# Performance work log

Hardware: AMD Instinct MI355X
Metric: run time of the kernel (lower is better)

Reference implementation:

```python
import jax, jax.numpy as jnp
import numpy as np

NEG_SLOPE = 0.2


def _gat_layer(x, src, dst, W, att_src, att_dst, bias, heads, out_c, concat):
    # x: [N, F_in]; src,dst: [E] (edges src -> dst, softmax grouped by dst)
    N = x.shape[0]
    h = (x @ W).reshape(N, heads, out_c)                       # [N,H,C]
    a_s = jnp.sum(h * att_src, axis=-1)                        # [N,H]
    a_d = jnp.sum(h * att_dst, axis=-1)                        # [N,H]
    e = jax.nn.leaky_relu(a_s[src] + a_d[dst], NEG_SLOPE)      # [E,H]
    emax = jax.ops.segment_max(e, dst, num_segments=N)         # [N,H]
    ex = jnp.exp(e - emax[dst])
    denom = jax.ops.segment_sum(ex, dst, num_segments=N)       # [N,H]
    alpha = ex / (denom[dst] + 1e-16)                          # [E,H]
    msg = h[src] * alpha[:, :, None]                           # [E,H,C]
    out = jax.ops.segment_sum(msg, dst, num_segments=N)        # [N,H,C]
    out = out.reshape(N, heads * out_c) if concat else out.mean(axis=1)
    return out + bias


def setup_inputs() -> dict:
    key = jax.random.key(0)
    ks = jax.random.split(key, 12)
    N, E = 100000, 1600000
    F_in, C1, H = 128, 32, 4
    x = jax.random.normal(ks[0], (N, F_in), dtype=jnp.float32)
    edge_index = jax.random.randint(ks[1], (2, E), 0, N, dtype=jnp.int64)
    s = 0.1
    W1 = jax.random.normal(ks[2], (F_in, H * C1), dtype=jnp.float32) * s
    att_src1 = jax.random.normal(ks[3], (H, C1), dtype=jnp.float32) * s
    att_dst1 = jax.random.normal(ks[4], (H, C1), dtype=jnp.float32) * s
    b1 = jnp.zeros((H * C1,), dtype=jnp.float32)
    W2 = jax.random.normal(ks[5], (H * C1, 1), dtype=jnp.float32) * s
    att_src2 = jax.random.normal(ks[6], (1, 1), dtype=jnp.float32) * s
    att_dst2 = jax.random.normal(ks[7], (1, 1), dtype=jnp.float32) * s
    b2 = jnp.zeros((1,), dtype=jnp.float32)
    return {"x": x, "edge_index": edge_index, "W1": W1, "att_src1": att_src1,
            "att_dst1": att_dst1, "b1": b1, "W2": W2, "att_src2": att_src2,
            "att_dst2": att_dst2, "b2": b2}


def reference(x, edge_index, W1, att_src1, att_dst1, b1, W2, att_src2, att_dst2, b2):
    N = x.shape[0]
    # PyG GATConv adds self loops by default
    loops = jnp.arange(N, dtype=edge_index.dtype)
    src = jnp.concatenate([edge_index[0], loops])
    dst = jnp.concatenate([edge_index[1], loops])
    h = _gat_layer(x, src, dst, W1, att_src1, att_dst1, b1, heads=4, out_c=32, concat=True)
    h = jax.nn.relu(h)
    out = _gat_layer(h, src, dst, W2, att_src2, att_dst2, b2, heads=1, out_c=1, concat=False)
    return out.squeeze(-1)  # [N]
```

## Files before the change

kernel.cpp:

```cpp
#include <hip/hip_runtime.h>
#include <hip/hip_bf16.h>
#include <math.h>

typedef __hip_bfloat16 bf16;
typedef __attribute__((ext_vector_type(8))) short short8v;
typedef __attribute__((ext_vector_type(4))) float float4v;

__device__ __forceinline__ float b2f(bf16 v) { return __bfloat162float(v); }
__device__ __forceinline__ float bs2f(unsigned short s) {
    unsigned u = ((unsigned)s) << 16;
    float f; __builtin_memcpy(&f, &u, 4); return f;
}
__device__ __forceinline__ short f2bs(float v) {
    bf16 b = __float2bfloat16(v);
    short s; __builtin_memcpy(&s, &b, 2); return s;
}
__device__ __forceinline__ float lrelu(float v) { return v > 0.f ? v : 0.2f * v; }
__device__ __forceinline__ float ldf(const void* p, size_t i, int bf) {
    return bf ? b2f(((const bf16*)p)[i]) : ((const float*)p)[i];
}
__device__ __forceinline__ int ld_src(const int* ei, int e, int E, int f64, int N) {
    int v = f64 ? (int)(((const long long*)ei)[e]) : ei[e];
    if ((unsigned)v >= (unsigned)N) v = 0;
    return v;
}
__device__ __forceinline__ int ld_dst(const int* ei, int e, int E, int f64, int N) {
    int v = f64 ? (int)(((const long long*)ei)[(size_t)E + e]) : ei[(size_t)E + e];
    if ((unsigned)v >= (unsigned)N) v = 0;
    return v;
}

#define EPB 4096
#define SB  8

__global__ void k_detect(const int* __restrict__ ei, const unsigned* __restrict__ xw,
                         int* __restrict__ flags, int* __restrict__ bcnt, int nbuck)
{
    __shared__ int s_or[256];
    __shared__ int s_cnt[256];
    int t = threadIdx.x;
    for (int j = t; j < nbuck; j += 256) bcnt[j] = 0;
    int any = 0, cnt = 0;
    for (int i = t; i < 4096; i += 256) {
        any |= ei[2 * i + 1];
        unsigned e = (xw[i] >> 7) & 0xFFu;
        cnt += (e >= 100u && e <= 134u) ? 1 : 0;
    }
    s_or[t] = any; s_cnt[t] = cnt;
    __syncthreads();
    for (int s = 128; s > 0; s >>= 1) {
        if (t < s) { s_or[t] |= s_or[t + s]; s_cnt[t] += s_cnt[t + s]; }
        __syncthreads();
    }
    if (t == 0) {
        flags[0] = (s_or[0] == 0) ? 1 : 0;
        flags[1] = (s_cnt[0] > 2048) ? 1 : 0;
    }
}

__global__ void __launch_bounds__(256)
k_prep(const int* __restrict__ ei, const void* __restrict__ W1,
       const int* __restrict__ flags, int* __restrict__ bcnt,
       short* __restrict__ w1frag, int E, int N, int nbuck, int ebl)
{
    int t = threadIdx.x;
    if (blockIdx.x >= ebl) {
        int bf = flags[1];
        int idx = (blockIdx.x - ebl) * 256 + t;
        if (idx < 16384) {
            int j = idx & 7, l = (idx >> 3) & 63, kk = (idx >> 9) & 3, ct = idx >> 11;
            int k = kk * 32 + (l >> 4) * 8 + j;
            int n = ct * 16 + (l & 15);
            w1frag[idx] = bf ? ((const short*)W1)[k * 128 + n]
                             : f2bs(((const float*)W1)[k * 128 + n]);
        }
        return;
    }
    __shared__ int hist[512];
    for (int j = t; j < nbuck; j += 256) hist[j] = 0;
    __syncthreads();
    int f = flags[0];
    int beg = blockIdx.x * EPB, end = min(E, beg + EPB);
    for (int i = beg + t; i < end; i += 256)
        atomicAdd(&hist[ld_dst(ei, i, E, f, N) >> SB], 1);
    __syncthreads();
    for (int j = t; j < nbuck; j += 256)
        if (hist[j]) atomicAdd(&bcnt[j], hist[j]);
}

#define GP 136

__global__ void __launch_bounds__(256)
k_gemm_scan(const void* __restrict__ x, const short* __restrict__ w1frag,
            const void* __restrict__ att_src, const void* __restrict__ att_dst,
            const int* __restrict__ flags, bf16* __restrict__ h1b,
            float* __restrict__ a_s, float* __restrict__ a_d,
            const int* __restrict__ bcnt, int* __restrict__ bofs,
            int* __restrict__ bcur, int* __restrict__ offsets,
            int N, int E, int nbuck)
{
    int t = threadIdx.x;
    if (blockIdx.x == 0) {
        __shared__ int ps[256];
        int i0 = 2 * t, i1 = 2 * t + 1;
        int c0 = (i0 < nbuck) ? bcnt[i0] : 0;
        int c1 = (i1 < nbuck) ? bcnt[i1] : 0;
        int pr = c0 + c1;
        ps[t] = pr;
        __syncthreads();
        for (int s = 1; s < 256; s <<= 1) {
            int add = (t >= s) ? ps[t - s] : 0;
            __syncthreads();
            ps[t] += add;
            __syncthreads();
        }
        int excl = ps[t] - pr;
        if (i0 < nbuck) { bofs[i0] = excl; bcur[i0] = excl; }
        if (i1 < nbuck) { bofs[i1] = excl + c0; bcur[i1] = excl + c0; }
        if (t == 0) { bofs[nbuck] = E; offsets[N] = E; }
        return;
    }
    __shared__ short xs[64 * GP];
    int bf = flags[1];
    int blk = blockIdx.x - 1;
    int base = blk * 64;
    if (bf) {
        const short8v* xp = (const short8v*)x;
        for (int idx = t; idx < 1024; idx += 256) {
            int m = idx >> 4, v8 = idx & 15;
            int gm = base + m;
            short8v v = (gm < N) ? xp[(size_t)gm * 16 + v8]
                                 : (short8v){0,0,0,0,0,0,0,0};
            *(short8v*)&xs[m * GP + v8 * 8] = v;
        }
    } else {
        const float4* xp = (const float4*)x;
        for (int idx = t; idx < 2048; idx += 256) {
            int m = idx >> 5, v4 = idx & 31;
            int gm = base + m;
            float4 f = (gm < N) ? xp[(size_t)gm * 32 + v4]
                                : make_float4(0.f, 0.f, 0.f, 0.f);
            short* d = &xs[m * GP + v4 * 4];
            d[0] = f2bs(f.x); d[1] = f2bs(f.y); d[2] = f2bs(f.z); d[3] = f2bs(f.w);
        }
    }
    __syncthreads();

    int wv = t >> 6, l = t & 63, lq = l >> 4, lr = l & 15;
    int m0 = base + wv * 16;

    short8v afr[4];
#pragma unroll
    for (int kk = 0; kk < 4; ++kk)
        afr[kk] = *(const short8v*)&xs[(wv * 16 + lr) * GP + kk * 32 + lq * 8];

    float4v acc[8];
#pragma unroll
    for (int ct = 0; ct < 8; ++ct) acc[ct] = (float4v){0.f, 0.f, 0.f, 0.f};

#pragma unroll
    for (int kk = 0; kk < 4; ++kk) {
        short8v a = afr[kk];
#pragma unroll
        for (int ct = 0; ct < 8; ++ct) {
            short8v b = *(const short8v*)(w1frag + (((ct * 4 + kk) * 64 + l) << 3));
            acc[ct] = __builtin_amdgcn_mfma_f32_16x16x32_bf16(a, b, acc[ct], 0, 0, 0);
        }
    }
    __syncthreads();

#pragma unroll
    for (int ct = 0; ct < 8; ++ct)
#pragma unroll
        for (int r = 0; r < 4; ++r)
            xs[(wv * 16 + lq * 4 + r) * GP + ct * 16 + lr] = f2bs(acc[ct][r]);
    __syncthreads();

    int c0 = (l & 7) * 16;
    float asv[16], adv[16];
#pragma unroll
    for (int c = 0; c < 16; ++c) {
        asv[c] = ldf(att_src, c0 + c, bf);
        adv[c] = ldf(att_dst, c0 + c, bf);
    }
#pragma unroll
    for (int p = 0; p < 2; ++p) {
        int rrow = p * 8 + (l >> 3);
        int gn = m0 + rrow;
        const short* srcp = &xs[(wv * 16 + rrow) * GP + c0];
        short8v v0 = *(const short8v*)srcp;
        short8v v1 = *(const short8v*)(srcp + 8);
        if (gn < N) {
            unsigned short* dst = (unsigned short*)h1b + (size_t)gn * 128 + c0;
            *(short8v*)dst = v0;
            *(short8v*)(dst + 8) = v1;
        }
        float ds = 0.f, dd = 0.f;
#pragma unroll
        for (int c = 0; c < 8; ++c) {
            float fv = bs2f((unsigned short)v0[c]);
            ds += fv * asv[c]; dd += fv * adv[c];
        }
#pragma unroll
        for (int c = 0; c < 8; ++c) {
            float fv = bs2f((unsigned short)v1[c]);
            ds += fv * asv[8 + c]; dd += fv * adv[8 + c];
        }
        ds += __shfl_xor(ds, 1, 64);
        dd += __shfl_xor(dd, 1, 64);
        if (gn < N && ((l & 1) == 0)) {
            int h = (l & 7) >> 1;
            a_s[(size_t)gn * 4 + h] = ds;
            a_d[(size_t)gn * 4 + h] = dd;
        }
    }
}

__global__ void __launch_bounds__(256)
k_bbin_scatter(const int* __restrict__ ei, const int* __restrict__ flags,
               int* __restrict__ bcur, uint2* __restrict__ ebuf,
               int E, int N, int nbuck)
{
    __shared__ int hist[512];
    __shared__ int base[512];
    int t = threadIdx.x;
    for (int j = t; j < nbuck; j += 256) hist[j] = 0;
    __syncthreads();
    int f = flags[0];
    int beg = blockIdx.x * EPB, end = min(E, beg + EPB);
    for (int i = beg + t; i < end; i += 256)
        atomicAdd(&hist[ld_dst(ei, i, E, f, N) >> SB], 1);
    __syncthreads();
    for (int j = t; j < nbuck; j += 256) {
        base[j] = hist[j] ? atomicAdd(&bcur[j], hist[j]) : 0;
        hist[j] = 0;
    }
    __syncthreads();
    for (int i = beg + t; i < end; i += 256) {
        int d = ld_dst(ei, i, E, f, N);
        int s = ld_src(ei, i, E, f, N);
        int b = d >> SB;
        int idx = base[b] + atomicAdd(&hist[b], 1);
        ebuf[idx] = make_uint2((unsigned)s, (unsigned)d);
    }
}

__global__ void __launch_bounds__(256)
k_bucket_csr(const uint2* __restrict__ ebuf, const int* __restrict__ bofs,
             int* __restrict__ offsets, int* __restrict__ adj, int N)
{
    const int npb = 1 << SB;
    __shared__ int hist[npb];
    __shared__ int psum[256];
    int b = blockIdx.x, t = threadIdx.x;
    int n0 = b << SB;
    int ebeg = bofs[b], eend = bofs[b + 1];

    hist[t] = 0;
    __syncthreads();
    for (int i = ebeg + t; i < eend; i += 256)
        atomicAdd(&hist[ebuf[i].y - n0], 1);
    __syncthreads();
    int c = hist[t];
    psum[t] = c;
    __syncthreads();
    for (int st = 1; st < 256; st <<= 1) {
        int add = (t >= st) ? psum[t - st] : 0;
        __syncthreads();
        psum[t] += add;
        __syncthreads();
    }
    int run = ebeg + psum[t] - c;
    int node = n0 + t;
    hist[t] = run;
    if (node < N) offsets[node] = run;
    __syncthreads();
    for (int i = ebeg + t; i < eend; i += 256) {
        uint2 e = ebuf[i];
        int pos = atomicAdd(&hist[e.y - n0], 1);
        adj[pos] = (int)e.x;
    }
}

__global__ void __launch_bounds__(256)
k_hagg32(const bf16* __restrict__ h1b, const float* __restrict__ a_s,
         const float* __restrict__ a_d, const int* __restrict__ offsets,
         const int* __restrict__ adj, const void* __restrict__ b1,
         const void* __restrict__ W2, const int* __restrict__ flags,
         float* __restrict__ h2, int N)
{
    int bf = flags[1];
    int t = threadIdx.x;
    int g = t >> 5, l = t & 31;
    int n = blockIdx.x * 8 + g;
    if (n >= N) return;
    int h = l >> 3;
    int coff = h * 32 + (l & 7) * 4;

    int beg = offsets[n], deg = offsets[n + 1] - beg;
    float adh = a_d[(size_t)n * 4 + h];
    const unsigned short* h1u = (const unsigned short*)h1b;

    float wself = __expf(lrelu(a_s[(size_t)n * 4 + h] + adh));
    ushort4 u = *(const ushort4*)(h1u + ((size_t)n << 7) + coff);
    float a0 = wself * bs2f(u.x), a1 = wself * bs2f(u.y);
    float a2 = wself * bs2f(u.z), a3 = wself * bs2f(u.w);
    float den = wself;

    int i = 0;
    for (; i + 4 <= deg; i += 4) {
        int s0 = adj[beg + i];
        int s1 = adj[beg + i + 1];
        int s2 = adj[beg + i + 2];
        int s3 = adj[beg + i + 3];
        float w0 = __expf(lrelu(a_s[(size_t)s0 * 4 + h] + adh));
        float w1 = __expf(lrelu(a_s[(size_t)s1 * 4 + h] + adh));
        float w2 = __expf(lrelu(a_s[(size_t)s2 * 4 + h] + adh));
        float w3 = __expf(lrelu(a_s[(size_t)s3 * 4 + h] + adh));
        ushort4 v0 = *(const ushort4*)(h1u + ((size_t)s0 << 7) + coff);
        ushort4 v1 = *(const ushort4*)(h1u + ((size_t)s1 << 7) + coff);
        ushort4 v2 = *(const ushort4*)(h1u + ((size_t)s2 << 7) + coff);
        ushort4 v3 = *(const ushort4*)(h1u + ((size_t)s3 << 7) + coff);
        den += (w0 + w1) + (w2 + w3);
        a0 += w0 * bs2f(v0.x) + w1 * bs2f(v1.x) + w2 * bs2f(v2.x) + w3 * bs2f(v3.x);
        a1 += w0 * bs2f(v0.y) + w1 * bs2f(v1.y) + w2 * bs2f(v2.y) + w3 * bs2f(v3.y);
        a2 += w0 * bs2f(v0.z) + w1 * bs2f(v1.z) + w2 * bs2f(v2.z) + w3 * bs2f(v3.z);
        a3 += w0 * bs2f(v0.w) + w1 * bs2f(v1.w) + w2 * bs2f(v2.w) + w3 * bs2f(v3.w);
    }
    for (; i < deg; ++i) {
        int s0 = adj[beg + i];
        float w0 = __expf(lrelu(a_s[(size_t)s0 * 4 + h] + adh));
        ushort4 v0 = *(const ushort4*)(h1u + ((size_t)s0 << 7) + coff);
        den += w0;
        a0 += w0 * bs2f(v0.x);
        a1 += w0 * bs2f(v0.y);
        a2 += w0 * bs2f(v0.z);
        a3 += w0 * bs2f(v0.w);
    }

    float inv = 1.f / (den + 1e-16f);
    float o0 = fmaxf(a0 * inv + ldf(b1, coff + 0, bf), 0.f);
    float o1 = fmaxf(a1 * inv + ldf(b1, coff + 1, bf), 0.f);
    float o2 = fmaxf(a2 * inv + ldf(b1, coff + 2, bf), 0.f);
    float o3 = fmaxf(a3 * inv + ldf(b1, coff + 3, bf), 0.f);

    float p = o0 * ldf(W2, coff + 0, bf) + o1 * ldf(W2, coff + 1, bf)
            + o2 * ldf(W2, coff + 2, bf) + o3 * ldf(W2, coff + 3, bf);
    p += __shfl_xor(p, 1, 64);
    p += __shfl_xor(p, 2, 64);
    p += __shfl_xor(p, 4, 64);
    p += __shfl_xor(p, 8, 64);
    p += __shfl_xor(p, 16, 64);
    if (l == 0) h2[n] = p;
}

__global__ void k_agg2(const float* __restrict__ h2, const int* __restrict__ offsets,
                       const int* __restrict__ adj, const void* __restrict__ att_src2,
                       const void* __restrict__ att_dst2, const void* __restrict__ bias2,
                       const int* __restrict__ flags, void* __restrict__ out, int N)
{
    int bf = flags[1];
    int g = (blockIdx.x * blockDim.x + threadIdx.x) >> 4;
    int lane = threadIdx.x & 15;
    if (g >= N) return;
    int n = g;
    float as2 = ldf(att_src2, 0, bf), ad2 = ldf(att_dst2, 0, bf);
    int beg = offsets[n], end = offsets[n + 1], deg = end - beg;
    float hn = h2[n];
    float dterm = hn * ad2;

    float acc = 0.f, den = 0.f;
    if (lane == 0) {
        float ex = __expf(lrelu(hn * as2 + dterm));
        acc = ex * hn; den = ex;
    }
    for (int i = lane; i < deg; i += 16) {
        int s = adj[beg + i];
        float hs = h2[s];
        float ex = __expf(lrelu(hs * as2 + dterm));
        acc += ex * hs; den += ex;
    }
    for (int m = 1; m < 16; m <<= 1) {
        acc += __shfl_xor(acc, m, 64);
        den += __shfl_xor(den, m, 64);
    }
    if (lane == 0) {
        float r = acc / (den + 1e-16f) + ldf(bias2, 0, bf);
        if (bf) ((bf16*)out)[n] = __float2bfloat16(r);
        else    ((float*)out)[n] = r;
    }
}

extern "C" void kernel_launch(void* const* d_in, const int* in_sizes, int n_in,
                              void* d_out, int out_size, void* d_ws, size_t ws_size,
                              hipStream_t stream)
{
    const void* x        = d_in[0];
    const int*  ei       = (const int*)d_in[1];
    const void* W1       = d_in[2];
    const void* att_src1 = d_in[3];
    const void* att_dst1 = d_in[4];
    const void* b1       = d_in[5];
    const void* W2       = d_in[6];
    const void* att_src2 = d_in[7];
    const void* att_dst2 = d_in[8];
    const void* bias2    = d_in[9];

    int N = in_sizes[0] / 128;
    int E = in_sizes[1] / 2;
    int nbuck = ((N - 1) >> SB) + 1;

    char* ws = (char*)d_ws;
    size_t off = 0;
    auto alloc = [&](size_t bytes) -> void* {
        void* p = ws + off;
        off = (off + bytes + 255) & ~(size_t)255;
        return p;
    };
    int*   flags   = (int*)alloc(256);
    float* a_s     = (float*)alloc((size_t)N * 4 * sizeof(float));
    float* a_d     = (float*)alloc((size_t)N * 4 * sizeof(float));
    float* h2      = (float*)alloc((size_t)N * sizeof(float));
    int*   offsets = (int*)alloc((size_t)(N + 1) * sizeof(int));
    int*   adj     = (int*)alloc((size_t)E * sizeof(int));
    uint2* ebuf    = (uint2*)alloc((size_t)E * sizeof(uint2));
    int*   bcnt    = (int*)alloc(1024 * sizeof(int));
    int*   bofs    = (int*)alloc(1028 * sizeof(int));
    int*   bcur    = (int*)alloc(1024 * sizeof(int));
    short* w1frag  = (short*)alloc(16384 * sizeof(short));
    bf16*  h1b     = (bf16*)alloc((size_t)N * 128 * sizeof(bf16));

    int ebl = (E + EPB - 1) / EPB;

    k_detect<<<1, 256, 0, stream>>>(ei, (const unsigned*)x, flags, bcnt, nbuck);

    k_prep<<<ebl + 64, 256, 0, stream>>>(ei, W1, flags, bcnt, w1frag,
                                         E, N, nbuck, ebl);

    k_gemm_scan<<<1 + (N + 63) / 64, 256, 0, stream>>>(
        x, w1frag, att_src1, att_dst1, flags, h1b, a_s, a_d,
        bcnt, bofs, bcur, offsets, N, E, nbuck);

    k_bbin_scatter<<<ebl, 256, 0, stream>>>(ei, flags, bcur, ebuf, E, N, nbuck);
    k_bucket_csr<<<nbuck, 256, 0, stream>>>(ebuf, bofs, offsets, adj, N);

    k_hagg32<<<(N + 7) / 8, 256, 0, stream>>>(h1b, a_s, a_d, offsets, adj,
                                              b1, W2, flags, h2, N);

    k_agg2<<<((size_t)N * 16 + 255) / 256, 256, 0, stream>>>(
        h2, offsets, adj, att_src2, att_dst2, bias2, flags, d_out, N);
}
```

Baseline: 279.9 us.

## Pack edge buffer into 32-bit words and aggregate with 16 lanes per node

The bucketed edge buffer now stores each edge as one 32-bit word, with the 24-bit source index and the 8-bit local destination index packed together, instead of a uint2. This halves traffic for the scatter and CSR-build passes. The layer-1 aggregation kernel now gives each node 16 lanes, each doing a 16-byte load of 8 bf16 channels and accumulating with packed float2 math, so twice as many nodes fit per block. The packing assumes N stays below 2^24, and each lane now needs more registers.

```diff
diff --git a/kernel.cpp b/kernel.cpp
--- a/kernel.cpp
+++ b/kernel.cpp
@@ -5,17 +5,21 @@
 typedef __hip_bfloat16 bf16;
 typedef __attribute__((ext_vector_type(8))) short short8v;
 typedef __attribute__((ext_vector_type(4))) float float4v;
+typedef __attribute__((ext_vector_type(2))) float float2v;
 
 __device__ __forceinline__ float b2f(bf16 v) { return __bfloat162float(v); }
 __device__ __forceinline__ float bs2f(unsigned short s) {
     unsigned u = ((unsigned)s) << 16;
     float f; __builtin_memcpy(&f, &u, 4); return f;
 }
+__device__ __forceinline__ float ubits(unsigned u) {
+    float f; __builtin_memcpy(&f, &u, 4); return f;
+}
 __device__ __forceinline__ short f2bs(float v) {
     bf16 b = __float2bfloat16(v);
     short s; __builtin_memcpy(&s, &b, 2); return s;
 }
-__device__ __forceinline__ float lrelu(float v) { return v > 0.f ? v : 0.2f * v; }
+__device__ __forceinline__ float lrelu(float v) { return fmaxf(v, 0.2f * v); }
 __device__ __forceinline__ float ldf(const void* p, size_t i, int bf) {
     return bf ? b2f(((const bf16*)p)[i]) : ((const float*)p)[i];
 }
@@ -218,7 +222,7 @@
 
 __global__ void __launch_bounds__(256)
 k_bbin_scatter(const int* __restrict__ ei, const int* __restrict__ flags,
-               int* __restrict__ bcur, uint2* __restrict__ ebuf,
+               int* __restrict__ bcur, unsigned* __restrict__ ebuf,
                int E, int N, int nbuck)
 {
     __shared__ int hist[512];
@@ -241,12 +245,12 @@
         int s = ld_src(ei, i, E, f, N);
         int b = d >> SB;
         int idx = base[b] + atomicAdd(&hist[b], 1);
-        ebuf[idx] = make_uint2((unsigned)s, (unsigned)d);
+        ebuf[idx] = (unsigned)s | ((unsigned)(d & ((1 << SB) - 1)) << 24);
     }
 }
 
 __global__ void __launch_bounds__(256)
-k_bucket_csr(const uint2* __restrict__ ebuf, const int* __restrict__ bofs,
+k_bucket_csr(const unsigned* __restrict__ ebuf, const int* __restrict__ bofs,
              int* __restrict__ offsets, int* __restrict__ adj, int N)
 {
     const int npb = 1 << SB;
@@ -259,7 +263,7 @@
     hist[t] = 0;
     __syncthreads();
     for (int i = ebeg + t; i < eend; i += 256)
-        atomicAdd(&hist[ebuf[i].y - n0], 1);
+        atomicAdd(&hist[ebuf[i] >> 24], 1);
     __syncthreads();
     int c = hist[t];
     psum[t] = c;
@@ -276,14 +280,25 @@
     if (node < N) offsets[node] = run;
     __syncthreads();
     for (int i = ebeg + t; i < eend; i += 256) {
-        uint2 e = ebuf[i];
-        int pos = atomicAdd(&hist[e.y - n0], 1);
-        adj[pos] = (int)e.x;
-    }
+        unsigned e = ebuf[i];
+        int pos = atomicAdd(&hist[e >> 24], 1);
+        adj[pos] = (int)(e & 0xFFFFFFu);
+    }
+}
+
+__device__ __forceinline__ void acc8(float2v& p0, float2v& p1, float2v& p2,
+                                     float2v& p3, uint4 q, float w)
+{
+    float2v wv = {w, w};
+    float2v v;
+    v[0] = ubits(q.x << 16); v[1] = ubits(q.x & 0xFFFF0000u); p0 += wv * v;
+    v[0] = ubits(q.y << 16); v[1] = ubits(q.y & 0xFFFF0000u); p1 += wv * v;
+    v[0] = ubits(q.z << 16); v[1] = ubits(q.z & 0xFFFF0000u); p2 += wv * v;
+    v[0] = ubits(q.w << 16); v[1] = ubits(q.w & 0xFFFF0000u); p3 += wv * v;
 }
 
 __global__ void __launch_bounds__(256)
-k_hagg32(const bf16* __restrict__ h1b, const float* __restrict__ a_s,
+k_hagg16(const bf16* __restrict__ h1b, const float* __restrict__ a_s,
          const float* __restrict__ a_d, const int* __restrict__ offsets,
          const int* __restrict__ adj, const void* __restrict__ b1,
          const void* __restrict__ W2, const int* __restrict__ flags,
@@ -291,22 +306,25 @@
 {
     int bf = flags[1];
     int t = threadIdx.x;
-    int g = t >> 5, l = t & 31;
-    int n = blockIdx.x * 8 + g;
+    int g = t >> 4, l = t & 15;
+    int n = blockIdx.x * 16 + g;
     if (n >= N) return;
-    int h = l >> 3;
-    int coff = h * 32 + (l & 7) * 4;
+    int h = l >> 2;
+    int c0 = l * 8;
+    const unsigned* h1q = (const unsigned*)h1b;
+    size_t rowsh = 6;
 
     int beg = offsets[n], deg = offsets[n + 1] - beg;
     float adh = a_d[(size_t)n * 4 + h];
-    const unsigned short* h1u = (const unsigned short*)h1b;
-
-    float wself = __expf(lrelu(a_s[(size_t)n * 4 + h] + adh));
-    ushort4 u = *(const ushort4*)(h1u + ((size_t)n << 7) + coff);
-    float a0 = wself * bs2f(u.x), a1 = wself * bs2f(u.y);
-    float a2 = wself * bs2f(u.z), a3 = wself * bs2f(u.w);
-    float den = wself;
-
+
+    float2v p0 = {0.f,0.f}, p1 = {0.f,0.f}, p2 = {0.f,0.f}, p3 = {0.f,0.f};
+    float den;
+    {
+        float w = __expf(lrelu(a_s[(size_t)n * 4 + h] + adh));
+        uint4 q = *(const uint4*)(h1q + ((size_t)n << rowsh) + l * 4);
+        acc8(p0, p1, p2, p3, q, w);
+        den = w;
+    }
     int i = 0;
     for (; i + 4 <= deg; i += 4) {
         int s0 = adj[beg + i];
@@ -317,40 +335,36 @@
         float w1 = __expf(lrelu(a_s[(size_t)s1 * 4 + h] + adh));
         float w2 = __expf(lrelu(a_s[(size_t)s2 * 4 + h] + adh));
         float w3 = __expf(lrelu(a_s[(size_t)s3 * 4 + h] + adh));
-        ushort4 v0 = *(const ushort4*)(h1u + ((size_t)s0 << 7) + coff);
-        ushort4 v1 = *(const ushort4*)(h1u + ((size_t)s1 << 7) + coff);
-        ushort4 v2 = *(const ushort4*)(h1u + ((size_t)s2 << 7) + coff);
-        ushort4 v3 = *(const ushort4*)(h1u + ((size_t)s3 << 7) + coff);
+        uint4 q0 = *(const uint4*)(h1q + ((size_t)s0 << rowsh) + l * 4);
+        uint4 q1 = *(const uint4*)(h1q + ((size_t)s1 << rowsh) + l * 4);
+        uint4 q2 = *(const uint4*)(h1q + ((size_t)s2 << rowsh) + l * 4);
+        uint4 q3 = *(const uint4*)(h1q + ((size_t)s3 << rowsh) + l * 4);
         den += (w0 + w1) + (w2 + w3);
-        a0 += w0 * bs2f(v0.x) + w1 * bs2f(v1.x) + w2 * bs2f(v2.x) + w3 * bs2f(v3.x);
-        a1 += w0 * bs2f(v0.y) + w1 * bs2f(v1.y) + w2 * bs2f(v2.y) + w3 * bs2f(v3.y);
-        a2 += w0 * bs2f(v0.z) + w1 * bs2f(v1.z) + w2 * bs2f(v2.z) + w3 * bs2f(v3.z);
-        a3 += w0 * bs2f(v0.w) + w1 * bs2f(v1.w) + w2 * bs2f(v2.w) + w3 * bs2f(v3.w);
+        acc8(p0, p1, p2, p3, q0, w0);
+        acc8(p0, p1, p2, p3, q1, w1);
+        acc8(p0, p1, p2, p3, q2, w2);
+        acc8(p0, p1, p2, p3, q3, w3);
     }
     for (; i < deg; ++i) {
         int s0 = adj[beg + i];
         float w0 = __expf(lrelu(a_s[(size_t)s0 * 4 + h] + adh));
-        ushort4 v0 = *(const ushort4*)(h1u + ((size_t)s0 << 7) + coff);
+        uint4 q0 = *(const uint4*)(h1q + ((size_t)s0 << rowsh) + l * 4);
         den += w0;
-        a0 += w0 * bs2f(v0.x);
-        a1 += w0 * bs2f(v0.y);
-        a2 += w0 * bs2f(v0.z);
-        a3 += w0 * bs2f(v0.w);
+        acc8(p0, p1, p2, p3, q0, w0);
     }
 
     float inv = 1.f / (den + 1e-16f);
-    float o0 = fmaxf(a0 * inv + ldf(b1, coff + 0, bf), 0.f);
-    float o1 = fmaxf(a1 * inv + ldf(b1, coff + 1, bf), 0.f);
-    float o2 = fmaxf(a2 * inv + ldf(b1, coff + 2, bf), 0.f);
-    float o3 = fmaxf(a3 * inv + ldf(b1, coff + 3, bf), 0.f);
-
-    float p = o0 * ldf(W2, coff + 0, bf) + o1 * ldf(W2, coff + 1, bf)
-            + o2 * ldf(W2, coff + 2, bf) + o3 * ldf(W2, coff + 3, bf);
+    float o[8] = { p0[0], p0[1], p1[0], p1[1], p2[0], p2[1], p3[0], p3[1] };
+    float p = 0.f;
+#pragma unroll
+    for (int c = 0; c < 8; ++c) {
+        float ov = fmaxf(o[c] * inv + ldf(b1, c0 + c, bf), 0.f);
+        p += ov * ldf(W2, c0 + c, bf);
+    }
     p += __shfl_xor(p, 1, 64);
     p += __shfl_xor(p, 2, 64);
     p += __shfl_xor(p, 4, 64);
     p += __shfl_xor(p, 8, 64);
-    p += __shfl_xor(p, 16, 64);
     if (l == 0) h2[n] = p;
 }
 
@@ -417,18 +431,18 @@
         off = (off + bytes + 255) & ~(size_t)255;
         return p;
     };
-    int*   flags   = (int*)alloc(256);
-    float* a_s     = (float*)alloc((size_t)N * 4 * sizeof(float));
-    float* a_d     = (float*)alloc((size_t)N * 4 * sizeof(float));
-    float* h2      = (float*)alloc((size_t)N * sizeof(float));
-    int*   offsets = (int*)alloc((size_t)(N + 1) * sizeof(int));
-    int*   adj     = (int*)alloc((size_t)E * sizeof(int));
-    uint2* ebuf    = (uint2*)alloc((size_t)E * sizeof(uint2));
-    int*   bcnt    = (int*)alloc(1024 * sizeof(int));
-    int*   bofs    = (int*)alloc(1028 * sizeof(int));
-    int*   bcur    = (int*)alloc(1024 * sizeof(int));
-    short* w1frag  = (short*)alloc(16384 * sizeof(short));
-    bf16*  h1b     = (bf16*)alloc((size_t)N * 128 * sizeof(bf16));
+    int*      flags   = (int*)alloc(256);
+    float*    a_s     = (float*)alloc((size_t)N * 4 * sizeof(float));
+    float*    a_d     = (float*)alloc((size_t)N * 4 * sizeof(float));
+    float*    h2      = (float*)alloc((size_t)N * sizeof(float));
+    int*      offsets = (int*)alloc((size_t)(N + 1) * sizeof(int));
+    int*      adj     = (int*)alloc((size_t)E * sizeof(int));
+    unsigned* ebuf    = (unsigned*)alloc((size_t)E * sizeof(unsigned));
+    int*      bcnt    = (int*)alloc(1024 * sizeof(int));
+    int*      bofs    = (int*)alloc(1028 * sizeof(int));
+    int*      bcur    = (int*)alloc(1024 * sizeof(int));
+    short*    w1frag  = (short*)alloc(16384 * sizeof(short));
+    bf16*     h1b     = (bf16*)alloc((size_t)N * 128 * sizeof(bf16));
 
     int ebl = (E + EPB - 1) / EPB;
 
@@ -444,8 +458,8 @@
     k_bbin_scatter<<<ebl, 256, 0, stream>>>(ei, flags, bcur, ebuf, E, N, nbuck);
     k_bucket_csr<<<nbuck, 256, 0, stream>>>(ebuf, bofs, offsets, adj, N);
 
-    k_hagg32<<<(N + 7) / 8, 256, 0, stream>>>(h1b, a_s, a_d, offsets, adj,
-                                              b1, W2, flags, h2, N);
+    k_hagg16<<<(N + 15) / 16, 256, 0, stream>>>(h1b, a_s, a_d, offsets, adj,
+                                                b1, W2, flags, h2, N);
 
     k_agg2<<<((size_t)N * 16 + 255) / 256, 256, 0, stream>>>(
         h2, offsets, adj, att_src2, att_dst2, bias2, flags, d_out, N);
```

After: 287.8 us. 2.8% more time.

## Fuse bucket scan into histogram and scatter into GEMM; pack edges to 32-bit

Applied to the files above, without the earlier changes.

The bucket prefix scan now runs in the last-finishing block of the histogram kernel, detected with an atomic counter. The edge bucket-scatter is merged into the GEMM kernel as extra blocks, which removes one launch and lets the scatter overlap with the GEMM. Edge records are packed into one 32-bit word (24-bit source, 8-bit local destination), halving ebuf traffic. The aggregation loop gains an 8-way unrolled gather for more memory-level parallelism, and leaky-ReLU uses fmaxf. The packing assumes N fits in 24 bits, and the last-block scan relies on threadfence ordering.

```diff
diff --git a/kernel.cpp b/kernel.cpp
--- a/kernel.cpp
+++ b/kernel.cpp
@@ -15,7 +15,7 @@
     bf16 b = __float2bfloat16(v);
     short s; __builtin_memcpy(&s, &b, 2); return s;
 }
-__device__ __forceinline__ float lrelu(float v) { return v > 0.f ? v : 0.2f * v; }
+__device__ __forceinline__ float lrelu(float v) { return fmaxf(v, 0.2f * v); }
 __device__ __forceinline__ float ldf(const void* p, size_t i, int bf) {
     return bf ? b2f(((const bf16*)p)[i]) : ((const float*)p)[i];
 }
@@ -34,12 +34,14 @@
 #define SB  8
 
 __global__ void k_detect(const int* __restrict__ ei, const unsigned* __restrict__ xw,
-                         int* __restrict__ flags, int* __restrict__ bcnt, int nbuck)
+                         int* __restrict__ flags, int* __restrict__ bcnt,
+                         int* __restrict__ done, int nbuck)
 {
     __shared__ int s_or[256];
     __shared__ int s_cnt[256];
     int t = threadIdx.x;
     for (int j = t; j < nbuck; j += 256) bcnt[j] = 0;
+    if (t == 0) done[0] = 0;
     int any = 0, cnt = 0;
     for (int i = t; i < 4096; i += 256) {
         any |= ei[2 * i + 1];
@@ -61,7 +63,9 @@
 __global__ void __launch_bounds__(256)
 k_prep(const int* __restrict__ ei, const void* __restrict__ W1,
        const int* __restrict__ flags, int* __restrict__ bcnt,
-       short* __restrict__ w1frag, int E, int N, int nbuck, int ebl)
+       short* __restrict__ w1frag, int* __restrict__ done,
+       int* __restrict__ bofs, int* __restrict__ bcur, int* __restrict__ offsets,
+       int E, int N, int nbuck, int ebl)
 {
     int t = threadIdx.x;
     if (blockIdx.x >= ebl) {
@@ -86,44 +90,70 @@
     __syncthreads();
     for (int j = t; j < nbuck; j += 256)
         if (hist[j]) atomicAdd(&bcnt[j], hist[j]);
+
+    __threadfence();
+    __shared__ int is_last;
+    if (t == 0) is_last = (atomicAdd(done, 1) == ebl - 1) ? 1 : 0;
+    __syncthreads();
+    if (!is_last) return;
+    __threadfence();
+    __shared__ int ps[256];
+    int i0 = 2 * t, i1 = 2 * t + 1;
+    int c0 = (i0 < nbuck) ? bcnt[i0] : 0;
+    int c1 = (i1 < nbuck) ? bcnt[i1] : 0;
+    int pr = c0 + c1;
+    ps[t] = pr;
+    __syncthreads();
+    for (int s = 1; s < 256; s <<= 1) {
+        int add = (t >= s) ? ps[t - s] : 0;
+        __syncthreads();
+        ps[t] += add;
+        __syncthreads();
+    }
+    int excl = ps[t] - pr;
+    if (i0 < nbuck) { bofs[i0] = excl; bcur[i0] = excl; }
+    if (i1 < nbuck) { bofs[i1] = excl + c0; bcur[i1] = excl + c0; }
+    if (t == 0) { bofs[nbuck] = E; offsets[N] = E; }
 }
 
 #define GP 136
 
 __global__ void __launch_bounds__(256)
-k_gemm_scan(const void* __restrict__ x, const short* __restrict__ w1frag,
-            const void* __restrict__ att_src, const void* __restrict__ att_dst,
-            const int* __restrict__ flags, bf16* __restrict__ h1b,
-            float* __restrict__ a_s, float* __restrict__ a_d,
-            const int* __restrict__ bcnt, int* __restrict__ bofs,
-            int* __restrict__ bcur, int* __restrict__ offsets,
-            int N, int E, int nbuck)
+k_gemm_scatter(const void* __restrict__ x, const short* __restrict__ w1frag,
+               const void* __restrict__ att_src, const void* __restrict__ att_dst,
+               const int* __restrict__ ei, const int* __restrict__ flags,
+               bf16* __restrict__ h1b, float* __restrict__ a_s, float* __restrict__ a_d,
+               int* __restrict__ bcur, unsigned* __restrict__ ebuf,
+               int N, int E, int nbuck, int ebl)
 {
     int t = threadIdx.x;
-    if (blockIdx.x == 0) {
-        __shared__ int ps[256];
-        int i0 = 2 * t, i1 = 2 * t + 1;
-        int c0 = (i0 < nbuck) ? bcnt[i0] : 0;
-        int c1 = (i1 < nbuck) ? bcnt[i1] : 0;
-        int pr = c0 + c1;
-        ps[t] = pr;
-        __syncthreads();
-        for (int s = 1; s < 256; s <<= 1) {
-            int add = (t >= s) ? ps[t - s] : 0;
-            __syncthreads();
-            ps[t] += add;
-            __syncthreads();
-        }
-        int excl = ps[t] - pr;
-        if (i0 < nbuck) { bofs[i0] = excl; bcur[i0] = excl; }
-        if (i1 < nbuck) { bofs[i1] = excl + c0; bcur[i1] = excl + c0; }
-        if (t == 0) { bofs[nbuck] = E; offsets[N] = E; }
+    if (blockIdx.x < ebl) {
+        __shared__ int hist[512];
+        __shared__ int base[512];
+        for (int j = t; j < nbuck; j += 256) hist[j] = 0;
+        __syncthreads();
+        int f = flags[0];
+        int beg = blockIdx.x * EPB, end = min(E, beg + EPB);
+        for (int i = beg + t; i < end; i += 256)
+            atomicAdd(&hist[ld_dst(ei, i, E, f, N) >> SB], 1);
+        __syncthreads();
+        for (int j = t; j < nbuck; j += 256) {
+            base[j] = hist[j] ? atomicAdd(&bcur[j], hist[j]) : 0;
+            hist[j] = 0;
+        }
+        __syncthreads();
+        for (int i = beg + t; i < end; i += 256) {
+            int d = ld_dst(ei, i, E, f, N);
+            int s = ld_src(ei, i, E, f, N);
+            int b = d >> SB;
+            int idx = base[b] + atomicAdd(&hist[b], 1);
+            ebuf[idx] = (unsigned)s | ((unsigned)(d & ((1 << SB) - 1)) << 24);
+        }
         return;
     }
     __shared__ short xs[64 * GP];
     int bf = flags[1];
-    int blk = blockIdx.x - 1;
-    int base = blk * 64;
+    int base = (blockIdx.x - ebl) * 64;
     if (bf) {
         const short8v* xp = (const short8v*)x;
         for (int idx = t; idx < 1024; idx += 256) {
@@ -217,36 +247,7 @@
 }
 
 __global__ void __launch_bounds__(256)
-k_bbin_scatter(const int* __restrict__ ei, const int* __restrict__ flags,
-               int* __restrict__ bcur, uint2* __restrict__ ebuf,
-               int E, int N, int nbuck)
-{
-    __shared__ int hist[512];
-    __shared__ int base[512];
-    int t = threadIdx.x;
-    for (int j = t; j < nbuck; j += 256) hist[j] = 0;
-    __syncthreads();
-    int f = flags[0];
-    int beg = blockIdx.x * EPB, end = min(E, beg + EPB);
-    for (int i = beg + t; i < end; i += 256)
-        atomicAdd(&hist[ld_dst(ei, i, E, f, N) >> SB], 1);
-    __syncthreads();
-    for (int j = t; j < nbuck; j += 256) {
-        base[j] = hist[j] ? atomicAdd(&bcur[j], hist[j]) : 0;
-        hist[j] = 0;
-    }
-    __syncthreads();
-    for (int i = beg + t; i < end; i += 256) {
-        int d = ld_dst(ei, i, E, f, N);
-        int s = ld_src(ei, i, E, f, N);
-        int b = d >> SB;
-        int idx = base[b] + atomicAdd(&hist[b], 1);
-        ebuf[idx] = make_uint2((unsigned)s, (unsigned)d);
-    }
-}
-
-__global__ void __launch_bounds__(256)
-k_bucket_csr(const uint2* __restrict__ ebuf, const int* __restrict__ bofs,
+k_bucket_csr(const unsigned* __restrict__ ebuf, const int* __restrict__ bofs,
              int* __restrict__ offsets, int* __restrict__ adj, int N)
 {
     const int npb = 1 << SB;
@@ -259,7 +260,7 @@
     hist[t] = 0;
     __syncthreads();
     for (int i = ebeg + t; i < eend; i += 256)
-        atomicAdd(&hist[ebuf[i].y - n0], 1);
+        atomicAdd(&hist[ebuf[i] >> 24], 1);
     __syncthreads();
     int c = hist[t];
     psum[t] = c;
@@ -276,9 +277,9 @@
     if (node < N) offsets[node] = run;
     __syncthreads();
     for (int i = ebeg + t; i < eend; i += 256) {
-        uint2 e = ebuf[i];
-        int pos = atomicAdd(&hist[e.y - n0], 1);
-        adj[pos] = (int)e.x;
+        unsigned e = ebuf[i];
+        int pos = atomicAdd(&hist[e >> 24], 1);
+        adj[pos] = (int)(e & 0xFFFFFFu);
     }
 }
 
@@ -308,6 +309,27 @@
     float den = wself;
 
     int i = 0;
+    for (; i + 8 <= deg; i += 8) {
+        int sv[8];
+#pragma unroll
+        for (int j = 0; j < 8; ++j) sv[j] = adj[beg + i + j];
+        float wv[8];
+#pragma unroll
+        for (int j = 0; j < 8; ++j)
+            wv[j] = __expf(lrelu(a_s[(size_t)sv[j] * 4 + h] + adh));
+        ushort4 vv[8];
+#pragma unroll
+        for (int j = 0; j < 8; ++j)
+            vv[j] = *(const ushort4*)(h1u + ((size_t)sv[j] << 7) + coff);
+#pragma unroll
+        for (int j = 0; j < 8; ++j) {
+            den += wv[j];
+            a0 += wv[j] * bs2f(vv[j].x);
+            a1 += wv[j] * bs2f(vv[j].y);
+            a2 += wv[j] * bs2f(vv[j].z);
+            a3 += wv[j] * bs2f(vv[j].w);
+        }
+    }
     for (; i + 4 <= deg; i += 4) {
         int s0 = adj[beg + i];
         int s1 = adj[beg + i + 1];
@@ -417,31 +439,32 @@
         off = (off + bytes + 255) & ~(size_t)255;
         return p;
     };
-    int*   flags   = (int*)alloc(256);
-    float* a_s     = (float*)alloc((size_t)N * 4 * sizeof(float));
-    float* a_d     = (float*)alloc((size_t)N * 4 * sizeof(float));
-    float* h2      = (float*)alloc((size_t)N * sizeof(float));
-    int*   offsets = (int*)alloc((size_t)(N + 1) * sizeof(int));
-    int*   adj     = (int*)alloc((size_t)E * sizeof(int));
-    uint2* ebuf    = (uint2*)alloc((size_t)E * sizeof(uint2));
-    int*   bcnt    = (int*)alloc(1024 * sizeof(int));
-    int*   bofs    = (int*)alloc(1028 * sizeof(int));
-    int*   bcur    = (int*)alloc(1024 * sizeof(int));
-    short* w1frag  = (short*)alloc(16384 * sizeof(short));
-    bf16*  h1b     = (bf16*)alloc((size_t)N * 128 * sizeof(bf16));
+    int*      flags   = (int*)alloc(256);
+    int*      done    = (int*)alloc(256);
+    float*    a_s     = (float*)alloc((size_t)N * 4 * sizeof(float));
+    float*    a_d     = (float*)alloc((size_t)N * 4 * sizeof(float));
+    float*    h2      = (float*)alloc((size_t)N * sizeof(float));
+    int*      offsets = (int*)alloc((size_t)(N + 1) * sizeof(int));
+    int*      adj     = (int*)alloc((size_t)E * sizeof(int));
+    unsigned* ebuf    = (unsigned*)alloc((size_t)E * sizeof(unsigned));
+    int*      bcnt    = (int*)alloc(1024 * sizeof(int));
+    int*      bofs    = (int*)alloc(1028 * sizeof(int));
+    int*      bcur    = (int*)alloc(1024 * sizeof(int));
+    short*    w1frag  = (short*)alloc(16384 * sizeof(short));
+    bf16*     h1b     = (bf16*)alloc((size_t)N * 128 * sizeof(bf16));
 
     int ebl = (E + EPB - 1) / EPB;
-
-    k_detect<<<1, 256, 0, stream>>>(ei, (const unsigned*)x, flags, bcnt, nbuck);
-
-    k_prep<<<ebl + 64, 256, 0, stream>>>(ei, W1, flags, bcnt, w1frag,
-                                         E, N, nbuck, ebl);
-
-    k_gemm_scan<<<1 + (N + 63) / 64, 256, 0, stream>>>(
-        x, w1frag, att_src1, att_dst1, flags, h1b, a_s, a_d,
-        bcnt, bofs, bcur, offsets, N, E, nbuck);
-
-    k_bbin_scatter<<<ebl, 256, 0, stream>>>(ei, flags, bcur, ebuf, E, N, nbuck);
+    int gblocks = (N + 63) / 64;
+
+    k_detect<<<1, 256, 0, stream>>>(ei, (const unsigned*)x, flags, bcnt, done, nbuck);
+
+    k_prep<<<ebl + 64, 256, 0, stream>>>(ei, W1, flags, bcnt, w1frag, done,
+                                         bofs, bcur, offsets, E, N, nbuck, ebl);
+
+    k_gemm_scatter<<<ebl + gblocks, 256, 0, stream>>>(
+        x, w1frag, att_src1, att_dst1, ei, flags, h1b, a_s, a_d,
+        bcur, ebuf, N, E, nbuck, ebl);
+
     k_bucket_csr<<<nbuck, 256, 0, stream>>>(ebuf, bofs, offsets, adj, N);
 
     k_hagg32<<<(N + 7) / 8, 256, 0, stream>>>(h1b, a_s, a_d, offsets, adj,
```

Result: no change. 283.1 us (+1.1%).

## Pack edge buffer into 32-bit words and widen GEMM blocks to 128 rows

Applied to the files above, without the earlier changes.

The bucketed edge buffer now stores each edge as one 32-bit word: a 24-bit source index plus the 8-bit local destination offset, instead of a uint2 pair. This halves the bytes written by the scatter pass and read twice by the CSR-build pass. The fused GEMM/scan kernel now runs 512-thread blocks covering 128 rows each. The prefix scan in block 0 is guarded to the first 256 threads, which puts barriers inside a divergent branch. LeakyReLU is also rewritten as a single fmax.

```diff
diff --git a/kernel.cpp b/kernel.cpp
--- a/kernel.cpp
+++ b/kernel.cpp
@@ -15,7 +15,7 @@
     bf16 b = __float2bfloat16(v);
     short s; __builtin_memcpy(&s, &b, 2); return s;
 }
-__device__ __forceinline__ float lrelu(float v) { return v > 0.f ? v : 0.2f * v; }
+__device__ __forceinline__ float lrelu(float v) { return fmaxf(v, 0.2f * v); }
 __device__ __forceinline__ float ldf(const void* p, size_t i, int bf) {
     return bf ? b2f(((const bf16*)p)[i]) : ((const float*)p)[i];
 }
@@ -90,7 +90,7 @@
 
 #define GP 136
 
-__global__ void __launch_bounds__(256)
+__global__ void __launch_bounds__(512)
 k_gemm_scan(const void* __restrict__ x, const short* __restrict__ w1frag,
             const void* __restrict__ att_src, const void* __restrict__ att_dst,
             const int* __restrict__ flags, bf16* __restrict__ h1b,
@@ -102,31 +102,32 @@
     int t = threadIdx.x;
     if (blockIdx.x == 0) {
         __shared__ int ps[256];
-        int i0 = 2 * t, i1 = 2 * t + 1;
-        int c0 = (i0 < nbuck) ? bcnt[i0] : 0;
-        int c1 = (i1 < nbuck) ? bcnt[i1] : 0;
-        int pr = c0 + c1;
-        ps[t] = pr;
-        __syncthreads();
-        for (int s = 1; s < 256; s <<= 1) {
-            int add = (t >= s) ? ps[t - s] : 0;
+        if (t < 256) {
+            int i0 = 2 * t, i1 = 2 * t + 1;
+            int c0 = (i0 < nbuck) ? bcnt[i0] : 0;
+            int c1 = (i1 < nbuck) ? bcnt[i1] : 0;
+            int pr = c0 + c1;
+            ps[t] = pr;
             __syncthreads();
-            ps[t] += add;
-            __syncthreads();
-        }
-        int excl = ps[t] - pr;
-        if (i0 < nbuck) { bofs[i0] = excl; bcur[i0] = excl; }
-        if (i1 < nbuck) { bofs[i1] = excl + c0; bcur[i1] = excl + c0; }
-        if (t == 0) { bofs[nbuck] = E; offsets[N] = E; }
+            for (int s = 1; s < 256; s <<= 1) {
+                int add = (t >= s) ? ps[t - s] : 0;
+                __syncthreads();
+                ps[t] += add;
+                __syncthreads();
+            }
+            int excl = ps[t] - pr;
+            if (i0 < nbuck) { bofs[i0] = excl; bcur[i0] = excl; }
+            if (i1 < nbuck) { bofs[i1] = excl + c0; bcur[i1] = excl + c0; }
+            if (t == 0) { bofs[nbuck] = E; offsets[N] = E; }
+        }
         return;
     }
-    __shared__ short xs[64 * GP];
+    __shared__ short xs[128 * GP];
     int bf = flags[1];
-    int blk = blockIdx.x - 1;
-    int base = blk * 64;
+    int base = (blockIdx.x - 1) * 128;
     if (bf) {
         const short8v* xp = (const short8v*)x;
-        for (int idx = t; idx < 1024; idx += 256) {
+        for (int idx = t; idx < 2048; idx += 512) {
             int m = idx >> 4, v8 = idx & 15;
             int gm = base + m;
             short8v v = (gm < N) ? xp[(size_t)gm * 16 + v8]
@@ -135,7 +136,7 @@
         }
     } else {
         const float4* xp = (const float4*)x;
-        for (int idx = t; idx < 2048; idx += 256) {
+        for (int idx = t; idx < 4096; idx += 512) {
             int m = idx >> 5, v4 = idx & 31;
             int gm = base + m;
             float4 f = (gm < N) ? xp[(size_t)gm * 32 + v4]
@@ -217,9 +218,9 @@
 }
 
 __global__ void __launch_bounds__(256)
-k_bbin_scatter(const int* __restrict__ ei, const int* __restrict__ flags,
-               int* __restrict__ bcur, uint2* __restrict__ ebuf,
-               int E, int N, int nbuck)
+k_scatter(const int* __restrict__ ei, const int* __restrict__ flags,
+          int* __restrict__ bcur, unsigned* __restrict__ ebuf,
+          int E, int N, int nbuck)
 {
     __shared__ int hist[512];
     __shared__ int base[512];
@@ -241,12 +242,12 @@
         int s = ld_src(ei, i, E, f, N);
         int b = d >> SB;
         int idx = base[b] + atomicAdd(&hist[b], 1);
-        ebuf[idx] = make_uint2((unsigned)s, (unsigned)d);
+        ebuf[idx] = (unsigned)s | ((unsigned)(d & ((1 << SB) - 1)) << 24);
     }
 }
 
 __global__ void __launch_bounds__(256)
-k_bucket_csr(const uint2* __restrict__ ebuf, const int* __restrict__ bofs,
+k_bucket_csr(const unsigned* __restrict__ ebuf, const int* __restrict__ bofs,
              int* __restrict__ offsets, int* __restrict__ adj, int N)
 {
     const int npb = 1 << SB;
@@ -259,7 +260,7 @@
     hist[t] = 0;
     __syncthreads();
     for (int i = ebeg + t; i < eend; i += 256)
-        atomicAdd(&hist[ebuf[i].y - n0], 1);
+        atomicAdd(&hist[ebuf[i] >> 24], 1);
     __syncthreads();
     int c = hist[t];
     psum[t] = c;
@@ -276,9 +277,9 @@
     if (node < N) offsets[node] = run;
     __syncthreads();
     for (int i = ebeg + t; i < eend; i += 256) {
-        uint2 e = ebuf[i];
-        int pos = atomicAdd(&hist[e.y - n0], 1);
-        adj[pos] = (int)e.x;
+        unsigned e = ebuf[i];
+        int pos = atomicAdd(&hist[e >> 24], 1);
+        adj[pos] = (int)(e & 0xFFFFFFu);
     }
 }
 
@@ -417,31 +418,33 @@
         off = (off + bytes + 255) & ~(size_t)255;
         return p;
     };
-    int*   flags   = (int*)alloc(256);
-    float* a_s     = (float*)alloc((size_t)N * 4 * sizeof(float));
-    float* a_d     = (float*)alloc((size_t)N * 4 * sizeof(float));
-    float* h2      = (float*)alloc((size_t)N * sizeof(float));
-    int*   offsets = (int*)alloc((size_t)(N + 1) * sizeof(int));
-    int*   adj     = (int*)alloc((size_t)E * sizeof(int));
-    uint2* ebuf    = (uint2*)alloc((size_t)E * sizeof(uint2));
-    int*   bcnt    = (int*)alloc(1024 * sizeof(int));
-    int*   bofs    = (int*)alloc(1028 * sizeof(int));
-    int*   bcur    = (int*)alloc(1024 * sizeof(int));
-    short* w1frag  = (short*)alloc(16384 * sizeof(short));
-    bf16*  h1b     = (bf16*)alloc((size_t)N * 128 * sizeof(bf16));
+    int*      flags   = (int*)alloc(256);
+    float*    a_s     = (float*)alloc((size_t)N * 4 * sizeof(float));
+    float*    a_d     = (float*)alloc((size_t)N * 4 * sizeof(float));
+    float*    h2      = (float*)alloc((size_t)N * sizeof(float));
+    int*      offsets = (int*)alloc((size_t)(N + 1) * sizeof(int));
+    int*      adj     = (int*)alloc((size_t)E * sizeof(int));
+    unsigned* ebuf    = (unsigned*)alloc((size_t)E * sizeof(unsigned));
+    int*      bcnt    = (int*)alloc(1024 * sizeof(int));
+    int*      bofs    = (int*)alloc(1028 * sizeof(int));
+    int*      bcur    = (int*)alloc(1024 * sizeof(int));
+    short*    w1frag  = (short*)alloc(16384 * sizeof(short));
+    bf16*     h1b     = (bf16*)alloc((size_t)N * 128 * sizeof(bf16));
 
     int ebl = (E + EPB - 1) / EPB;
+    int gblocks = (N + 127) / 128;
 
     k_detect<<<1, 256, 0, stream>>>(ei, (const unsigned*)x, flags, bcnt, nbuck);
 
     k_prep<<<ebl + 64, 256, 0, stream>>>(ei, W1, flags, bcnt, w1frag,
                                          E, N, nbuck, ebl);
 
-    k_gemm_scan<<<1 + (N + 63) / 64, 256, 0, stream>>>(
+    k_gemm_scan<<<1 + gblocks, 512, 0, stream>>>(
         x, w1frag, att_src1, att_dst1, flags, h1b, a_s, a_d,
         bcnt, bofs, bcur, offsets, N, E, nbuck);
 
-    k_bbin_scatter<<<ebl, 256, 0, stream>>>(ei, flags, bcur, ebuf, E, N, nbuck);
+    k_scatter<<<ebl, 256, 0, stream>>>(ei, flags, bcur, ebuf, E, N, nbuck);
+
     k_bucket_csr<<<nbuck, 256, 0, stream>>>(ebuf, bofs, offsets, adj, N);
 
     k_hagg32<<<(N + 7) / 8, 256, 0, stream>>>(h1b, a_s, a_d, offsets, adj,
```

New measurement: 283.2 us. Within noise of the previous version (+1.2%).
